# Kernel tuning notes

Hardware: AMD Instinct MI355X
Metric: run time of the kernel (lower is better)

Reference implementation:

```python
import jax, jax.numpy as jnp
import numpy as np

# SqueezeSeg CRF config
NUM_CLASS = 4
SIZE_Z, SIZE_A = 3, 5            # LCN_HEIGHT, LCN_WIDTH
B, H, W = 16, 64, 512            # batch, zenith, azimuth
RCRF_ITER = 3
BI_FILTER_COEF = 0.1
ANG_FILTER_COEF = 0.02
ANG_THETA_A = 0.9
BILATERAL_THETA_A = 0.9
K = SIZE_Z * SIZE_A              # 15 -> 14 neighbors (center excluded)

# neighbor offsets of the 3x5 condensing kernel, center excluded
OFFSETS = [(dz, da) for dz in range(SIZE_Z) for da in range(SIZE_A)
           if not (dz == SIZE_Z // 2 and da == SIZE_A // 2)]

def _gauss_weights(theta_sq):
    # angular_filter_kernel: Gaussian of squared spatial offset, center zeroed
    g = [np.exp(-((dz - SIZE_Z // 2) ** 2 + (da - SIZE_A // 2) ** 2) / (2.0 * theta_sq))
         for dz, da in OFFSETS]
    return jnp.asarray(np.array(g, dtype=np.float32))

def gather_neighbors(x):
    # x: [B,C,H,W] -> [B,C,K-1,H,W]; zero-padded 'same' neighborhood gather
    pz, pa = SIZE_Z // 2, SIZE_A // 2
    xp = jnp.pad(x, ((0, 0), (0, 0), (pz, pz), (pa, pa)))
    return jnp.stack([xp[:, :, dz:dz + H, da:da + W] for dz, da in OFFSETS], axis=2)

def setup_inputs() -> dict:
    key = jax.random.key(0)
    k1, k2, k3 = jax.random.split(key, 3)
    x = jax.random.normal(k1, (B, NUM_CLASS, H, W), dtype=jnp.float32)
    bilateral_filters = jax.random.uniform(k2, (B, 1, K - 1, H, W), dtype=jnp.float32)
    lidar_mask = (jax.random.uniform(k3, (B, 1, H, W)) > 0.5).astype(jnp.float32)
    return {"x": x, "bilateral_filters": bilateral_filters, "lidar_mask": lidar_mask}

def reference(x, bilateral_filters, lidar_mask):
    g_ang = _gauss_weights(ANG_THETA_A ** 2)
    g_bi = _gauss_weights(BILATERAL_THETA_A ** 2)
    compat = jnp.ones((NUM_CLASS, NUM_CLASS), jnp.float32) - jnp.eye(NUM_CLASS, dtype=jnp.float32)
    ang_compat = compat * ANG_FILTER_COEF   # [out_class, in_class] 1x1 conv
    bi_compat = compat * BI_FILTER_COEF

    for _ in range(RCRF_ITER):
        unary = jax.nn.softmax(x, axis=1)                     # softmax over class dim
        nb = gather_neighbors(unary)                          # [B,C,14,H,W]
        # depthwise angular filters = Gaussian-weighted neighbor sums
        ang = jnp.einsum('k,bckhw->bchw', g_ang, nb)
        bi_ang = jnp.einsum('k,bckhw->bchw', g_bi, nb)
        # condensing conv on masked unary, weighted by per-pixel bilateral filters
        nb_m = gather_neighbors(unary * lidar_mask)           # [B,C,14,H,W]
        condensed = jnp.sum(nb_m * bilateral_filters, axis=2) # [B,C,H,W]
        bi = condensed * lidar_mask * bi_ang
        # 1x1 compatibility transforms
        ang2 = jnp.einsum('oc,bchw->bohw', ang_compat, ang)
        bi2 = jnp.einsum('oc,bchw->bohw', bi_compat, bi)
        x = unary + ang2 + bi2
    return x
```

## Files before the change

### kernel.cpp

```cpp
#include <hip/hip_runtime.h>


#define NCLASS 4
#define HH 64
#define WW 512
#define BB 16
#define TH 8
#define TW 64
#define UR (TH + 6)
#define UC (TW + 12)
#define PLANE (HH * WW)

#define G1 0.53940412f
#define G2 0.29095687f
#define G4 0.08466190f
#define G5 0.04566227f

#define TAPS                                                                 \
    const int   DZ[14] = {-1,-1,-1,-1,-1,  0, 0, 0, 0,  1, 1, 1, 1, 1};      \
    const int   DA[14] = {-2,-1, 0, 1, 2, -2,-1, 1, 2, -2,-1, 0, 1, 2};      \
    const float GW[14] = {G5,G2,G1,G2,G5, G4,G1,G1,G4, G5,G2,G1,G2,G5};

template <int MR, int MC, bool FINAL>
__device__ __forceinline__ void crf_step(
    float4 (*__restrict__ u_lds)[UC], const float (*__restrict__ m_lds)[UC],
    const float* __restrict__ filt, float* __restrict__ dst,
    int b, int h0, int w0, int tid)
{
    constexpr int RH = TH + 2 * MR;
    constexpr int RW = TW + 2 * MC;
    constexpr int NS = (RH * RW + 255) / 256;
    TAPS

    float4 xnew[NS];

#pragma unroll
    for (int j = 0; j < NS; ++j) {
        const int s = tid + 256 * j;
        float4 r = make_float4(0.f, 0.f, 0.f, 0.f);
        if (s < RH * RW) {
            const int lr = s / RW;
            const int lc = s - lr * RW;
            const int gh = h0 + lr - MR;
            const int gw = w0 + lc - MC;
            const int ur = lr + (3 - MR);
            const int uc = lc + (6 - MC);
            if (gh >= 0 && gh < HH && gw >= 0 && gw < WW) {
                float a0 = 0.f, a1 = 0.f, a2 = 0.f, a3 = 0.f;
                float c0 = 0.f, c1 = 0.f, c2 = 0.f, c3 = 0.f;
                const float mcen = m_lds[ur][uc];
                const float* fp = filt + ((size_t)b * 14 * HH + gh) * WW + gw;
#pragma unroll
                for (int k = 0; k < 14; ++k) {
                    const float  f  = fp[(size_t)k * PLANE];
                    const float  mn = m_lds[ur + DZ[k]][uc + DA[k]];
                    const float4 u  = u_lds[ur + DZ[k]][uc + DA[k]];
                    const float  fm = f * mn;
                    const float  gk = GW[k];
                    a0 = fmaf(gk, u.x, a0);  c0 = fmaf(fm, u.x, c0);
                    a1 = fmaf(gk, u.y, a1);  c1 = fmaf(fm, u.y, c1);
                    a2 = fmaf(gk, u.z, a2);  c2 = fmaf(fm, u.z, c2);
                    a3 = fmaf(gk, u.w, a3);  c3 = fmaf(fm, u.w, c3);
                }
                const float b0 = c0 * mcen * a0;
                const float b1 = c1 * mcen * a1;
                const float b2 = c2 * mcen * a2;
                const float b3 = c3 * mcen * a3;
                const float sa = a0 + a1 + a2 + a3;
                const float sb = b0 + b1 + b2 + b3;
                const float4 ucen = u_lds[ur][uc];
                r.x = ucen.x + 0.02f * (sa - a0) + 0.1f * (sb - b0);
                r.y = ucen.y + 0.02f * (sa - a1) + 0.1f * (sb - b1);
                r.z = ucen.z + 0.02f * (sa - a2) + 0.1f * (sb - b2);
                r.w = ucen.w + 0.02f * (sa - a3) + 0.1f * (sb - b3);
                if (!FINAL) {
                    const float mx  = fmaxf(fmaxf(r.x, r.y), fmaxf(r.z, r.w));
                    const float e0  = __expf(r.x - mx);
                    const float e1  = __expf(r.y - mx);
                    const float e2  = __expf(r.z - mx);
                    const float e3  = __expf(r.w - mx);
                    const float inv = 1.0f / (e0 + e1 + e2 + e3);
                    r = make_float4(e0 * inv, e1 * inv, e2 * inv, e3 * inv);
                }
            }
            if (FINAL) {
                float* o = dst + ((size_t)b * NCLASS * HH + gh) * WW + gw;
                o[0]         = r.x;
                o[PLANE]     = r.y;
                o[2 * PLANE] = r.z;
                o[3 * PLANE] = r.w;
            }
        }
        if (!FINAL) xnew[j] = r;
    }

    if (!FINAL) {
        __syncthreads();
#pragma unroll
        for (int j = 0; j < NS; ++j) {
            const int s = tid + 256 * j;
            if (s < RH * RW) {
                const int lr = s / RW;
                const int lc = s - lr * RW;
                u_lds[lr + (3 - MR)][lc + (6 - MC)] = xnew[j];
            }
        }
        __syncthreads();
    }
}

__global__ __launch_bounds__(256, 4) void crf_fused(
    const float* __restrict__ xin,
    const float* __restrict__ filt,
    const float* __restrict__ mask,
    float* __restrict__ xout)
{
    __shared__ float4 u_lds[UR][UC];
    __shared__ float  m_lds[UR][UC];

    const int b   = blockIdx.z;
    const int h0  = blockIdx.y * TH;
    const int w0  = blockIdx.x * TW;
    const int tid = threadIdx.x;

    for (int idx = tid; idx < UR * UC; idx += 256) {
        const int lr = idx / UC;
        const int lc = idx - lr * UC;
        const int gh = h0 + lr - 3;
        const int gw = w0 + lc - 6;
        float4 u = make_float4(0.f, 0.f, 0.f, 0.f);
        float  m = 0.f;
        if (gh >= 0 && gh < HH && gw >= 0 && gw < WW) {
            const float* px = xin + ((size_t)b * NCLASS * HH + gh) * WW + gw;
            const float v0 = px[0];
            const float v1 = px[PLANE];
            const float v2 = px[2 * PLANE];
            const float v3 = px[3 * PLANE];
            const float mx = fmaxf(fmaxf(v0, v1), fmaxf(v2, v3));
            const float e0 = __expf(v0 - mx);
            const float e1 = __expf(v1 - mx);
            const float e2 = __expf(v2 - mx);
            const float e3 = __expf(v3 - mx);
            const float inv = 1.0f / (e0 + e1 + e2 + e3);
            u = make_float4(e0 * inv, e1 * inv, e2 * inv, e3 * inv);
            m = mask[((size_t)b * HH + gh) * WW + gw];
        }
        u_lds[lr][lc] = u;
        m_lds[lr][lc] = m;
    }
    __syncthreads();

    crf_step<2, 4, false>(u_lds, m_lds, filt, xout, b, h0, w0, tid);
    crf_step<1, 2, false>(u_lds, m_lds, filt, xout, b, h0, w0, tid);
    crf_step<0, 0, true >(u_lds, m_lds, filt, xout, b, h0, w0, tid);
}

extern "C" void kernel_launch(void* const* d_in, const int* in_sizes, int n_in,
                              void* d_out, int out_size, void* d_ws, size_t ws_size,
                              hipStream_t stream) {
    const float* x    = (const float*)d_in[0];
    const float* filt = (const float*)d_in[1];
    const float* msk  = (const float*)d_in[2];
    float* out = (float*)d_out;
    (void)d_ws; (void)ws_size;

    dim3 grid(WW / TW, HH / TH, BB);
    dim3 block(256);
    crf_fused<<<grid, block, 0, stream>>>(x, filt, msk, out);
}
```

Baseline: 100.7 us.

## Compute two adjacent pixels per thread with shared LDS window and float2 I/O

Each thread now handles two horizontally adjacent pixels. It loads a 6-wide row window of unary and mask values from LDS once and reuses it for both pixels' 14 taps, and it uses float2 vector loads and stores for the filter, input, mask and output. This is meant to cut LDS read traffic and global memory instruction count per pixel. In exchange it raises register pressure (14 float2 filter values plus several float4 accumulators), which may reduce occupancy under the 256x4 launch bounds.

```diff
diff --git a/kernel.cpp b/kernel.cpp
--- a/kernel.cpp
+++ b/kernel.cpp
@@ -16,10 +16,39 @@
 #define G4 0.08466190f
 #define G5 0.04566227f
 
-#define TAPS                                                                 \
-    const int   DZ[14] = {-1,-1,-1,-1,-1,  0, 0, 0, 0,  1, 1, 1, 1, 1};      \
-    const int   DA[14] = {-2,-1, 0, 1, 2, -2,-1, 1, 2, -2,-1, 0, 1, 2};      \
-    const float GW[14] = {G5,G2,G1,G2,G5, G4,G1,G1,G4, G5,G2,G1,G2,G5};
+__device__ __forceinline__ void fma4(float4& d, float s, const float4& v) {
+    d.x = fmaf(s, v.x, d.x);
+    d.y = fmaf(s, v.y, d.y);
+    d.z = fmaf(s, v.z, d.z);
+    d.w = fmaf(s, v.w, d.w);
+}
+
+template <bool SM>
+__device__ __forceinline__ float4 crf_combine(const float4 A, const float4 C,
+                                              const float4 u, const float mcen)
+{
+    const float bx = C.x * mcen * A.x;
+    const float by = C.y * mcen * A.y;
+    const float bz = C.z * mcen * A.z;
+    const float bw = C.w * mcen * A.w;
+    const float sa = A.x + A.y + A.z + A.w;
+    const float sb = bx + by + bz + bw;
+    float4 r;
+    r.x = u.x + 0.02f * (sa - A.x) + 0.1f * (sb - bx);
+    r.y = u.y + 0.02f * (sa - A.y) + 0.1f * (sb - by);
+    r.z = u.z + 0.02f * (sa - A.z) + 0.1f * (sb - bz);
+    r.w = u.w + 0.02f * (sa - A.w) + 0.1f * (sb - bw);
+    if (SM) {
+        const float mx  = fmaxf(fmaxf(r.x, r.y), fmaxf(r.z, r.w));
+        const float e0  = __expf(r.x - mx);
+        const float e1  = __expf(r.y - mx);
+        const float e2  = __expf(r.z - mx);
+        const float e3  = __expf(r.w - mx);
+        const float inv = 1.0f / (e0 + e1 + e2 + e3);
+        r = make_float4(e0 * inv, e1 * inv, e2 * inv, e3 * inv);
+    }
+    return r;
+}
 
 template <int MR, int MC, bool FINAL>
 __device__ __forceinline__ void crf_step(
@@ -27,71 +56,84 @@
     const float* __restrict__ filt, float* __restrict__ dst,
     int b, int h0, int w0, int tid)
 {
-    constexpr int RH = TH + 2 * MR;
-    constexpr int RW = TW + 2 * MC;
-    constexpr int NS = (RH * RW + 255) / 256;
-    TAPS
-
-    float4 xnew[NS];
+    constexpr int RH  = TH + 2 * MR;
+    constexpr int RW  = TW + 2 * MC;
+    constexpr int GPR = RW / 2;
+    constexpr int NG  = RH * GPR;
+    constexpr int NS  = (NG + 255) / 256;
+
+    const float GE[5] = {G5, G2, G1, G2, G5};
+    const float GC[5] = {G4, G1, 0.f, G1, G4};
+
+    float4 xa[NS], xb[NS];
 
 #pragma unroll
     for (int j = 0; j < NS; ++j) {
         const int s = tid + 256 * j;
-        float4 r = make_float4(0.f, 0.f, 0.f, 0.f);
-        if (s < RH * RW) {
-            const int lr = s / RW;
-            const int lc = s - lr * RW;
-            const int gh = h0 + lr - MR;
-            const int gw = w0 + lc - MC;
+        float4 r0 = make_float4(0.f, 0.f, 0.f, 0.f);
+        float4 r1 = make_float4(0.f, 0.f, 0.f, 0.f);
+        int gh = -1, gw = -1;
+        if (s < NG) {
+            const int lr = s / GPR;
+            const int gc = s - lr * GPR;
+            const int lc = 2 * gc;
+            gh = h0 + lr - MR;
+            gw = w0 + lc - MC;
             const int ur = lr + (3 - MR);
             const int uc = lc + (6 - MC);
             if (gh >= 0 && gh < HH && gw >= 0 && gw < WW) {
-                float a0 = 0.f, a1 = 0.f, a2 = 0.f, a3 = 0.f;
-                float c0 = 0.f, c1 = 0.f, c2 = 0.f, c3 = 0.f;
-                const float mcen = m_lds[ur][uc];
                 const float* fp = filt + ((size_t)b * 14 * HH + gh) * WW + gw;
-#pragma unroll
-                for (int k = 0; k < 14; ++k) {
-                    const float  f  = fp[(size_t)k * PLANE];
-                    const float  mn = m_lds[ur + DZ[k]][uc + DA[k]];
-                    const float4 u  = u_lds[ur + DZ[k]][uc + DA[k]];
-                    const float  fm = f * mn;
-                    const float  gk = GW[k];
-                    a0 = fmaf(gk, u.x, a0);  c0 = fmaf(fm, u.x, c0);
-                    a1 = fmaf(gk, u.y, a1);  c1 = fmaf(fm, u.y, c1);
-                    a2 = fmaf(gk, u.z, a2);  c2 = fmaf(fm, u.z, c2);
-                    a3 = fmaf(gk, u.w, a3);  c3 = fmaf(fm, u.w, c3);
+                float2 f[14];
+#pragma unroll
+                for (int k = 0; k < 14; ++k)
+                    f[k] = *reinterpret_cast<const float2*>(fp + (size_t)k * PLANE);
+
+                float4 A0 = make_float4(0.f, 0.f, 0.f, 0.f);
+                float4 A1 = A0, C0 = A0, C1 = A0;
+                float4 ucen0 = A0, ucen1 = A0;
+                float  mcen0 = 0.f, mcen1 = 0.f;
+
+#pragma unroll
+                for (int dz = -1; dz <= 1; ++dz) {
+                    const int rr = ur + dz;
+                    float4 U[6];
+                    float  M[6];
+#pragma unroll
+                    for (int t = 0; t < 6; ++t) U[t] = u_lds[rr][uc - 2 + t];
+#pragma unroll
+                    for (int t = 0; t < 3; ++t) {
+                        const float2 mm =
+                            *reinterpret_cast<const float2*>(&m_lds[rr][uc - 2 + 2 * t]);
+                        M[2 * t]     = mm.x;
+                        M[2 * t + 1] = mm.y;
+                    }
+                    if (dz == 0) { ucen0 = U[2]; ucen1 = U[3]; mcen0 = M[2]; mcen1 = M[3]; }
+#pragma unroll
+                    for (int t = 0; t < 5; ++t) {
+                        if (dz == 0 && t == 2) continue;
+                        const int   k  = (dz == -1) ? t
+                                       : (dz == 0)  ? 5 + (t > 2 ? t - 1 : t)
+                                                    : 9 + t;
+                        const float gk = (dz == 0) ? GC[t] : GE[t];
+                        const float fm0 = f[k].x * M[t];
+                        const float fm1 = f[k].y * M[t + 1];
+                        fma4(A0, gk,  U[t]);      fma4(C0, fm0, U[t]);
+                        fma4(A1, gk,  U[t + 1]);  fma4(C1, fm1, U[t + 1]);
+                    }
                 }
-                const float b0 = c0 * mcen * a0;
-                const float b1 = c1 * mcen * a1;
-                const float b2 = c2 * mcen * a2;
-                const float b3 = c3 * mcen * a3;
-                const float sa = a0 + a1 + a2 + a3;
-                const float sb = b0 + b1 + b2 + b3;
-                const float4 ucen = u_lds[ur][uc];
-                r.x = ucen.x + 0.02f * (sa - a0) + 0.1f * (sb - b0);
-                r.y = ucen.y + 0.02f * (sa - a1) + 0.1f * (sb - b1);
-                r.z = ucen.z + 0.02f * (sa - a2) + 0.1f * (sb - b2);
-                r.w = ucen.w + 0.02f * (sa - a3) + 0.1f * (sb - b3);
-                if (!FINAL) {
-                    const float mx  = fmaxf(fmaxf(r.x, r.y), fmaxf(r.z, r.w));
-                    const float e0  = __expf(r.x - mx);
-                    const float e1  = __expf(r.y - mx);
-                    const float e2  = __expf(r.z - mx);
-                    const float e3  = __expf(r.w - mx);
-                    const float inv = 1.0f / (e0 + e1 + e2 + e3);
-                    r = make_float4(e0 * inv, e1 * inv, e2 * inv, e3 * inv);
+                r0 = crf_combine<!FINAL>(A0, C0, ucen0, mcen0);
+                r1 = crf_combine<!FINAL>(A1, C1, ucen1, mcen1);
+
+                if (FINAL) {
+                    float* o = dst + ((size_t)b * NCLASS * HH + gh) * WW + gw;
+                    *reinterpret_cast<float2*>(o)             = make_float2(r0.x, r1.x);
+                    *reinterpret_cast<float2*>(o + PLANE)     = make_float2(r0.y, r1.y);
+                    *reinterpret_cast<float2*>(o + 2 * PLANE) = make_float2(r0.z, r1.z);
+                    *reinterpret_cast<float2*>(o + 3 * PLANE) = make_float2(r0.w, r1.w);
                 }
             }
-            if (FINAL) {
-                float* o = dst + ((size_t)b * NCLASS * HH + gh) * WW + gw;
-                o[0]         = r.x;
-                o[PLANE]     = r.y;
-                o[2 * PLANE] = r.z;
-                o[3 * PLANE] = r.w;
-            }
         }
-        if (!FINAL) xnew[j] = r;
+        if (!FINAL) { xa[j] = r0; xb[j] = r1; }
     }
 
     if (!FINAL) {
@@ -99,10 +141,12 @@
 #pragma unroll
         for (int j = 0; j < NS; ++j) {
             const int s = tid + 256 * j;
-            if (s < RH * RW) {
-                const int lr = s / RW;
-                const int lc = s - lr * RW;
-                u_lds[lr + (3 - MR)][lc + (6 - MC)] = xnew[j];
+            if (s < NG) {
+                const int lr = s / GPR;
+                const int gc = s - lr * GPR;
+                const int lc = 2 * gc;
+                u_lds[lr + (3 - MR)][lc + (6 - MC)]     = xa[j];
+                u_lds[lr + (3 - MR)][lc + (6 - MC) + 1] = xb[j];
             }
         }
         __syncthreads();
@@ -123,30 +167,44 @@
     const int w0  = blockIdx.x * TW;
     const int tid = threadIdx.x;
 
-    for (int idx = tid; idx < UR * UC; idx += 256) {
-        const int lr = idx / UC;
-        const int lc = idx - lr * UC;
+    constexpr int NP = (UR * UC) / 2;
+    for (int idx = tid; idx < NP; idx += 256) {
+        const int lr = idx / (UC / 2);
+        const int lc = 2 * (idx - lr * (UC / 2));
         const int gh = h0 + lr - 3;
         const int gw = w0 + lc - 6;
-        float4 u = make_float4(0.f, 0.f, 0.f, 0.f);
-        float  m = 0.f;
+        float4 u0 = make_float4(0.f, 0.f, 0.f, 0.f);
+        float4 u1 = u0;
+        float2 mm = make_float2(0.f, 0.f);
         if (gh >= 0 && gh < HH && gw >= 0 && gw < WW) {
             const float* px = xin + ((size_t)b * NCLASS * HH + gh) * WW + gw;
-            const float v0 = px[0];
-            const float v1 = px[PLANE];
-            const float v2 = px[2 * PLANE];
-            const float v3 = px[3 * PLANE];
-            const float mx = fmaxf(fmaxf(v0, v1), fmaxf(v2, v3));
-            const float e0 = __expf(v0 - mx);
-            const float e1 = __expf(v1 - mx);
-            const float e2 = __expf(v2 - mx);
-            const float e3 = __expf(v3 - mx);
-            const float inv = 1.0f / (e0 + e1 + e2 + e3);
-            u = make_float4(e0 * inv, e1 * inv, e2 * inv, e3 * inv);
-            m = mask[((size_t)b * HH + gh) * WW + gw];
+            const float2 v0 = *reinterpret_cast<const float2*>(px);
+            const float2 v1 = *reinterpret_cast<const float2*>(px + PLANE);
+            const float2 v2 = *reinterpret_cast<const float2*>(px + 2 * PLANE);
+            const float2 v3 = *reinterpret_cast<const float2*>(px + 3 * PLANE);
+            mm = *reinterpret_cast<const float2*>(mask + ((size_t)b * HH + gh) * WW + gw);
+            {
+                const float mx  = fmaxf(fmaxf(v0.x, v1.x), fmaxf(v2.x, v3.x));
+                const float e0  = __expf(v0.x - mx);
+                const float e1  = __expf(v1.x - mx);
+                const float e2  = __expf(v2.x - mx);
+                const float e3  = __expf(v3.x - mx);
+                const float inv = 1.0f / (e0 + e1 + e2 + e3);
+                u0 = make_float4(e0 * inv, e1 * inv, e2 * inv, e3 * inv);
+            }
+            {
+                const float mx  = fmaxf(fmaxf(v0.y, v1.y), fmaxf(v2.y, v3.y));
+                const float e0  = __expf(v0.y - mx);
+                const float e1  = __expf(v1.y - mx);
+                const float e2  = __expf(v2.y - mx);
+                const float e3  = __expf(v3.y - mx);
+                const float inv = 1.0f / (e0 + e1 + e2 + e3);
+                u1 = make_float4(e0 * inv, e1 * inv, e2 * inv, e3 * inv);
+            }
         }
-        u_lds[lr][lc] = u;
-        m_lds[lr][lc] = m;
+        u_lds[lr][lc]     = u0;
+        u_lds[lr][lc + 1] = u1;
+        *reinterpret_cast<float2*>(&m_lds[lr][lc]) = mm;
     }
     __syncthreads();
 
```

Measured after the change: 100.0 us. No clear change (-0.6%).
